# Kernel optimization log

Measured on AMD Instinct MI355X. Metric: run time of the kernel, lower is better.

The kernel has to match this reference:

```python
import jax, jax.numpy as jnp
import numpy as np

B, S, H, DH = 2, 4096, 8, 64
D = H * DH


def setup_inputs() -> dict:
    key = jax.random.key(0)
    ks = jax.random.split(key, 6)
    std = 1.0 / np.sqrt(D)
    return {
        "x": jax.random.normal(ks[0], (B, S, D), dtype=jnp.float32),
        "Wq": jax.random.normal(ks[1], (D, D), dtype=jnp.float32) * std,
        "Wk": jax.random.normal(ks[2], (D, D), dtype=jnp.float32) * std,
        "Wv": jax.random.normal(ks[3], (D, D), dtype=jnp.float32) * std,
        "Wo": jax.random.normal(ks[4], (D, D), dtype=jnp.float32) * std,
        "bo": jnp.zeros((D,), dtype=jnp.float32),
    }


def reference(x, Wq, Wk, Wv, Wo, bo):
    scale = DH ** (-0.5)
    # torch Linear: y = x @ W.T
    q = x @ Wq.T  # [B,S,D]
    k = x @ Wk.T
    v = x @ Wv.T
    # split heads -> [B,H,S,Dh]
    q = q.reshape(B, S, H, DH).transpose(0, 2, 1, 3)
    k = k.reshape(B, S, H, DH).transpose(0, 2, 1, 3)
    v = v.reshape(B, S, H, DH).transpose(0, 2, 1, 3)
    score = jnp.einsum('bhqd,bhkd->bhqk', q, k) * scale  # [B,H,S,S]
    weights = jax.nn.softmax(score, axis=-1)
    attn = jnp.einsum('bhqk,bhkd->bhqd', weights, v)  # [B,H,S,Dh]
    h_ = attn.transpose(0, 2, 1, 3).reshape(B, S, D)
    return h_ @ Wo.T + bo
```

## Files before the change

kernel.cpp:

```cpp
#include <hip/hip_runtime.h>

#define LOG2E 1.44269504088896340736f

typedef unsigned short u16;
typedef __bf16 bf16x4_t __attribute__((ext_vector_type(4)));
typedef __bf16 bf16x8_t __attribute__((ext_vector_type(8)));
typedef float f32x4_t __attribute__((ext_vector_type(4)));

__device__ __forceinline__ u16 f2bf(float f) {
  union { float f; unsigned int u; } v;
  v.f = f;
  unsigned int u = v.u;
  u += 0x7fffu + ((u >> 16) & 1u);
  return (u16)(u >> 16);
}

__device__ __forceinline__ f32x4_t mfma16(bf16x8_t a, bf16x8_t b, f32x4_t c) {
  return __builtin_amdgcn_mfma_f32_16x16x32_bf16(a, b, c, 0, 0, 0);
}

__device__ __forceinline__ void gl_lds16(const u16* g, u16* l) {
  __builtin_amdgcn_global_load_lds(
      (const __attribute__((address_space(1))) unsigned int*)g,
      (__attribute__((address_space(3))) unsigned int*)l, 16, 0, 0);
}

__global__ __launch_bounds__(256) void cast_all_kernel(
    const float* __restrict__ x, const float* __restrict__ wq, const float* __restrict__ wk,
    const float* __restrict__ wv, const float* __restrict__ wo,
    u16* __restrict__ xb, u16* __restrict__ wqb, u16* __restrict__ wkb,
    u16* __restrict__ wvb, u16* __restrict__ wob) {
  const int NX = 2 * 4096 * 512;
  const int NW = 512 * 512;
  int i = (blockIdx.x * 256 + threadIdx.x) * 4;
  const float* src; u16* dst; int off; float scale = 1.f;
  if (i < NX)               { src = x;  dst = xb;  off = i; }
  else if (i < NX + NW)     { src = wq; dst = wqb; off = i - NX; scale = 0.125f * LOG2E; }
  else if (i < NX + 2 * NW) { src = wk; dst = wkb; off = i - NX - NW; }
  else if (i < NX + 3 * NW) { src = wv; dst = wvb; off = i - NX - 2 * NW; }
  else                      { src = wo; dst = wob; off = i - NX - 3 * NW; }
  float4 f = *(const float4*)(src + off);
  unsigned int lo = (unsigned int)f2bf(f.x * scale) | ((unsigned int)f2bf(f.y * scale) << 16);
  unsigned int hi = (unsigned int)f2bf(f.z * scale) | ((unsigned int)f2bf(f.w * scale) << 16);
  uint2 o; o.x = lo; o.y = hi;
  *(uint2*)(dst + off) = o;
}

template <int MODE>
__device__ __forceinline__ void gemm_core(const u16* __restrict__ A, const u16* __restrict__ Bt,
                                          void* __restrict__ Cout, const float* __restrict__ bias,
                                          int Mbase, int Nbase) {
  __shared__ __align__(16) u16 As[128][40];
  __shared__ __align__(16) u16 Bs[128][40];
  const int t = threadIdx.x;
  const int wave = t >> 6, lane = t & 63;
  const int r = lane & 15, qd = lane >> 4;
  const int wm = wave & 1, wn = wave >> 1;
  const int lr = t >> 2;
  const int lc = (t & 3) * 8;

  f32x4_t acc[4][4];
#pragma unroll
  for (int i = 0; i < 4; i++)
#pragma unroll
    for (int j = 0; j < 4; j++) { f32x4_t z = {0.f, 0.f, 0.f, 0.f}; acc[i][j] = z; }

  for (int k0 = 0; k0 < 512; k0 += 32) {
    __syncthreads();
    *(uint4*)&As[lr][lc]      = *(const uint4*)(A  + (Mbase + lr) * 512 + k0 + lc);
    *(uint4*)&As[64 + lr][lc] = *(const uint4*)(A  + (Mbase + 64 + lr) * 512 + k0 + lc);
    *(uint4*)&Bs[lr][lc]      = *(const uint4*)(Bt + (Nbase + lr) * 512 + k0 + lc);
    *(uint4*)&Bs[64 + lr][lc] = *(const uint4*)(Bt + (Nbase + 64 + lr) * 512 + k0 + lc);
    __syncthreads();
    bf16x8_t af[4], bfr[4];
#pragma unroll
    for (int i = 0; i < 4; i++) af[i]  = *(const bf16x8_t*)&As[wm * 64 + i * 16 + r][qd * 8];
#pragma unroll
    for (int j = 0; j < 4; j++) bfr[j] = *(const bf16x8_t*)&Bs[wn * 64 + j * 16 + r][qd * 8];
#pragma unroll
    for (int i = 0; i < 4; i++)
#pragma unroll
      for (int j = 0; j < 4; j++) acc[i][j] = mfma16(af[i], bfr[j], acc[i][j]);
  }

  float bv[4];
  if (MODE == 2) {
#pragma unroll
    for (int j = 0; j < 4; j++) bv[j] = bias[Nbase + wn * 64 + j * 16 + r];
  }
#pragma unroll
  for (int i = 0; i < 4; i++) {
#pragma unroll
    for (int reg = 0; reg < 4; reg++) {
      int gr = Mbase + wm * 64 + i * 16 + qd * 4 + reg;
#pragma unroll
      for (int j = 0; j < 4; j++) {
        int gc = Nbase + wn * 64 + j * 16 + r;
        float val = acc[i][j][reg];
        if (MODE == 2) {
          ((float*)Cout)[gr * 512 + gc] = val + bv[j];
        } else if (MODE == 1) {
          int bb = gc >> 12, ss = gc & 4095;
          ((__bf16*)Cout)[((long)(bb * 512 + gr)) * 4096 + ss] = (__bf16)val;
        } else {
          ((__bf16*)Cout)[gr * 512 + gc] = (__bf16)val;
        }
      }
    }
  }
}

__global__ __launch_bounds__(256) void gemm_qkv_kernel(
    const u16* __restrict__ X,
    const u16* __restrict__ Wq, const u16* __restrict__ Wk, const u16* __restrict__ Wv,
    u16* __restrict__ Q, u16* __restrict__ K, u16* __restrict__ Vt) {
  if (blockIdx.z == 0)
    gemm_core<0>(X, Wq, Q, nullptr, blockIdx.x * 128, blockIdx.y * 128);
  else if (blockIdx.z == 1)
    gemm_core<0>(X, Wk, K, nullptr, blockIdx.x * 128, blockIdx.y * 128);
  else
    gemm_core<1>(Wv, X, Vt, nullptr, blockIdx.y * 128, blockIdx.x * 128);
}

__global__ __launch_bounds__(256) void gemm_out_kernel(
    const u16* __restrict__ Aat, const u16* __restrict__ Wo,
    float* __restrict__ Out, const float* __restrict__ bo) {
  gemm_core<2>(Aat, Wo, Out, bo, blockIdx.x * 128, blockIdx.y * 128);
}

__global__ __launch_bounds__(256, 2) void attn_kernel(
    const u16* __restrict__ Q, const u16* __restrict__ K, const u16* __restrict__ Vt,
    u16* __restrict__ Oattn) {
  __shared__ __align__(16) u16 Ks[2][4096];
  __shared__ __align__(16) u16 Vs[2][4096];
  __shared__ __align__(16) u16 Ps[4][4096];

  const int t = threadIdx.x;
  const int wave = t >> 6, lane = t & 63;
  const int r = lane & 15, qd = lane >> 4;
  const int g = wave & 1, kv = wave >> 1;
  const int bh = blockIdx.y;
  const int b = bh >> 3, h = bh & 7;
  const long bbase = (long)b * 4096 * 512;
  const int q0 = blockIdx.x * 128;

  const int sw = r & 7;
  const int ck0 = (qd ^ sw) * 8;
  const int ck1 = ((qd + 4) ^ sw) * 8;

  bf16x8_t qf[4][2];
#pragma unroll
  for (int qa = 0; qa < 4; qa++) {
    const u16* qp = Q + bbase + (long)(q0 + g * 64 + qa * 16 + r) * 512 + h * 64 + qd * 8;
    qf[qa][0] = *(const bf16x8_t*)(qp);
    qf[qa][1] = *(const bf16x8_t*)(qp + 32);
  }

  f32x4_t accO[4][4];
  float Lacc[4];
#pragma unroll
  for (int qa = 0; qa < 4; qa++) {
    f32x4_t z = {0.f, 0.f, 0.f, 0.f};
    Lacc[qa] = 0.f;
#pragma unroll
    for (int nt = 0; nt < 4; nt++) accO[qa][nt] = z;
  }

  const int rr = lane >> 3;
  const int cc = (lane & 7) ^ rr;
  const u16* kgb = K + bbase + (long)(kv * 2048 + g * 32 + rr) * 512 + h * 64 + cc * 8;
  const u16* vgb = Vt + ((long)(b * 512 + h * 64 + g * 32 + rr)) * 4096 + kv * 2048 + cc * 8;
  u16* kld = &Ks[kv][g * 32 * 64];
  u16* vld = &Vs[kv][g * 32 * 64];

  for (int k0 = 0; k0 < 2048; k0 += 64) {
    __syncthreads();
#pragma unroll
    for (int i = 0; i < 4; i++) gl_lds16(kgb + (long)k0 * 512 + i * 8 * 512, kld + i * 512);
#pragma unroll
    for (int i = 0; i < 4; i++) gl_lds16(vgb + k0 + i * 8 * 4096, vld + i * 512);
    __syncthreads();

    bf16x8_t kf[4][2];
#pragma unroll
    for (int nt = 0; nt < 4; nt++) {
      const u16* kb = &Ks[kv][(nt * 16 + r) * 64];
      kf[nt][0] = *(const bf16x8_t*)(kb + ck0);
      kf[nt][1] = *(const bf16x8_t*)(kb + ck1);
    }

    f32x4_t St[4][4];
#pragma unroll
    for (int qa = 0; qa < 4; qa++)
#pragma unroll
      for (int nt = 0; nt < 4; nt++) {
        f32x4_t z = {0.f, 0.f, 0.f, 0.f};
        z = mfma16(kf[nt][0], qf[qa][0], z);
        z = mfma16(kf[nt][1], qf[qa][1], z);
        St[qa][nt] = z;
      }

#pragma unroll
    for (int qa = 0; qa < 4; qa++) {
#pragma unroll
      for (int nt = 0; nt < 4; nt++) {
        float p0 = __builtin_amdgcn_exp2f(St[qa][nt][0]);
        float p1 = __builtin_amdgcn_exp2f(St[qa][nt][1]);
        float p2 = __builtin_amdgcn_exp2f(St[qa][nt][2]);
        float p3 = __builtin_amdgcn_exp2f(St[qa][nt][3]);
        Lacc[qa] += (p0 + p1) + (p2 + p3);
        bf16x4_t pk;
        pk[0] = (__bf16)p0; pk[1] = (__bf16)p1; pk[2] = (__bf16)p2; pk[3] = (__bf16)p3;
        int slot = (nt * 2 + (qd >> 1)) ^ sw;
        *(uint2*)&Ps[wave][(qa * 16 + r) * 64 + slot * 8 + (qd & 1) * 4] = *(uint2*)&pk;
      }
    }

    bf16x8_t pf[4][2];
#pragma unroll
    for (int qa = 0; qa < 4; qa++) {
      const u16* pb = &Ps[wave][(qa * 16 + r) * 64];
      pf[qa][0] = *(const bf16x8_t*)(pb + ck0);
      pf[qa][1] = *(const bf16x8_t*)(pb + ck1);
    }

#pragma unroll
    for (int nt = 0; nt < 4; nt++) {
      const u16* vb = &Vs[kv][(nt * 16 + r) * 64];
      bf16x8_t vf0 = *(const bf16x8_t*)(vb + ck0);
      bf16x8_t vf1 = *(const bf16x8_t*)(vb + ck1);
#pragma unroll
      for (int qa = 0; qa < 4; qa++) {
        accO[qa][nt] = mfma16(pf[qa][0], vf0, accO[qa][nt]);
        accO[qa][nt] = mfma16(pf[qa][1], vf1, accO[qa][nt]);
      }
    }
  }

  __syncthreads();
  float* Sc  = (float*)&Ps[0][0];
  float* Lsc = (float*)&Ks[0][0];
  if (kv == 1) {
#pragma unroll
    for (int qa = 0; qa < 4; qa++) {
#pragma unroll
      for (int nt = 0; nt < 4; nt++)
        *(f32x4_t*)&Sc[g * 4096 + ((qa * 4 + nt) * 64 + lane) * 4] = accO[qa][nt];
      Lsc[g * 256 + qa * 64 + lane] = Lacc[qa];
    }
  }
  __syncthreads();
  if (kv == 0) {
#pragma unroll
    for (int qa = 0; qa < 4; qa++) {
      Lacc[qa] += Lsc[g * 256 + qa * 64 + lane];
      float v = Lacc[qa];
      v += __shfl_xor(v, 16);
      v += __shfl_xor(v, 32);
      Lacc[qa] = v;
#pragma unroll
      for (int nt = 0; nt < 4; nt++) {
        f32x4_t o = *(const f32x4_t*)&Sc[g * 4096 + ((qa * 4 + nt) * 64 + lane) * 4];
        accO[qa][nt] += o;
      }
    }
#pragma unroll
    for (int qa = 0; qa < 4; qa++)
#pragma unroll
      for (int reg = 0; reg < 4; reg++) {
        float L = __shfl(Lacc[qa], qd * 4 + reg);
        float inv = 1.f / L;
        int gr = q0 + g * 64 + qa * 16 + qd * 4 + reg;
#pragma unroll
        for (int nt = 0; nt < 4; nt++)
          ((__bf16*)Oattn)[bbase + (long)gr * 512 + h * 64 + nt * 16 + r] =
              (__bf16)(accO[qa][nt][reg] * inv);
      }
  }
}

extern "C" void kernel_launch(void* const* d_in, const int* in_sizes, int n_in,
                              void* d_out, int out_size, void* d_ws, size_t ws_size,
                              hipStream_t stream) {
  const float* x  = (const float*)d_in[0];
  const float* Wq = (const float*)d_in[1];
  const float* Wk = (const float*)d_in[2];
  const float* Wv = (const float*)d_in[3];
  const float* Wo = (const float*)d_in[4];
  const float* bo = (const float*)d_in[5];
  float* out = (float*)d_out;

  u16* ws  = (u16*)d_ws;
  u16* xb  = ws;
  u16* wqb = xb  + 4194304;
  u16* wkb = wqb + 262144;
  u16* wvb = wkb + 262144;
  u16* wob = wvb + 262144;
  u16* Qb  = wob + 262144;
  u16* Kb  = Qb  + 4194304;
  u16* Vtg = Kb  + 4194304;
  u16* Ab  = Vtg + 4194304;

  cast_all_kernel<<<5120, 256, 0, stream>>>(x, Wq, Wk, Wv, Wo, xb, wqb, wkb, wvb, wob);

  dim3 g1(64, 4, 3);
  gemm_qkv_kernel<<<g1, 256, 0, stream>>>(xb, wqb, wkb, wvb, Qb, Kb, Vtg);

  dim3 g2(32, 16);
  attn_kernel<<<g2, 256, 0, stream>>>(Qb, Kb, Vtg, Ab);

  dim3 g3(64, 4);
  gemm_out_kernel<<<g3, 256, 0, stream>>>(Ab, wob, out, bo);
}
```

Before: 210.8 us.

## Double-buffer K/V tiles in attention and register-prefetch GEMM operands

The attention kernel now keeps two LDS buffers for the K and V tiles. It issues the async global-to-LDS loads for the next 64-key tile before computing on the current one, so there is one barrier per iteration instead of two. The per-wave P staging buffer is halved by writing and reading P in two 32-key halves interleaved with the PV MFMAs. The QKV and output GEMMs prefetch the next k-slice into registers while the current slice is multiplied from LDS. Together these aim to hide global load latency behind MFMA work. The cost is more LDS per block (80KB, still within two blocks per CU on 160KB) and more registers in the GEMM. Correctness depends on the async LDS loads having completed before the barrier.

```diff
diff --git a/kernel.cpp b/kernel.cpp
--- a/kernel.cpp
+++ b/kernel.cpp
@@ -65,22 +65,38 @@
 #pragma unroll
     for (int j = 0; j < 4; j++) { f32x4_t z = {0.f, 0.f, 0.f, 0.f}; acc[i][j] = z; }
 
+  const u16* pa0 = A  + (Mbase + lr) * 512 + lc;
+  const u16* pa1 = A  + (Mbase + 64 + lr) * 512 + lc;
+  const u16* pb0 = Bt + (Nbase + lr) * 512 + lc;
+  const u16* pb1 = Bt + (Nbase + 64 + lr) * 512 + lc;
+
+  uint4 ra0 = *(const uint4*)(pa0);
+  uint4 ra1 = *(const uint4*)(pa1);
+  uint4 rb0 = *(const uint4*)(pb0);
+  uint4 rb1 = *(const uint4*)(pb1);
+
   for (int k0 = 0; k0 < 512; k0 += 32) {
+    *(uint4*)&As[lr][lc]      = ra0;
+    *(uint4*)&As[64 + lr][lc] = ra1;
+    *(uint4*)&Bs[lr][lc]      = rb0;
+    *(uint4*)&Bs[64 + lr][lc] = rb1;
     __syncthreads();
-    *(uint4*)&As[lr][lc]      = *(const uint4*)(A  + (Mbase + lr) * 512 + k0 + lc);
-    *(uint4*)&As[64 + lr][lc] = *(const uint4*)(A  + (Mbase + 64 + lr) * 512 + k0 + lc);
-    *(uint4*)&Bs[lr][lc]      = *(const uint4*)(Bt + (Nbase + lr) * 512 + k0 + lc);
-    *(uint4*)&Bs[64 + lr][lc] = *(const uint4*)(Bt + (Nbase + 64 + lr) * 512 + k0 + lc);
+    if (k0 < 480) {
+      ra0 = *(const uint4*)(pa0 + k0 + 32);
+      ra1 = *(const uint4*)(pa1 + k0 + 32);
+      rb0 = *(const uint4*)(pb0 + k0 + 32);
+      rb1 = *(const uint4*)(pb1 + k0 + 32);
+    }
+    bf16x8_t af[4], bfr[4];
+#pragma unroll
+    for (int i = 0; i < 4; i++) af[i]  = *(const bf16x8_t*)&As[wm * 64 + i * 16 + r][qd * 8];
+#pragma unroll
+    for (int j = 0; j < 4; j++) bfr[j] = *(const bf16x8_t*)&Bs[wn * 64 + j * 16 + r][qd * 8];
+#pragma unroll
+    for (int i = 0; i < 4; i++)
+#pragma unroll
+      for (int j = 0; j < 4; j++) acc[i][j] = mfma16(af[i], bfr[j], acc[i][j]);
     __syncthreads();
-    bf16x8_t af[4], bfr[4];
-#pragma unroll
-    for (int i = 0; i < 4; i++) af[i]  = *(const bf16x8_t*)&As[wm * 64 + i * 16 + r][qd * 8];
-#pragma unroll
-    for (int j = 0; j < 4; j++) bfr[j] = *(const bf16x8_t*)&Bs[wn * 64 + j * 16 + r][qd * 8];
-#pragma unroll
-    for (int i = 0; i < 4; i++)
-#pragma unroll
-      for (int j = 0; j < 4; j++) acc[i][j] = mfma16(af[i], bfr[j], acc[i][j]);
   }
 
   float bv[4];
@@ -131,9 +147,9 @@
 __global__ __launch_bounds__(256, 2) void attn_kernel(
     const u16* __restrict__ Q, const u16* __restrict__ K, const u16* __restrict__ Vt,
     u16* __restrict__ Oattn) {
-  __shared__ __align__(16) u16 Ks[2][4096];
-  __shared__ __align__(16) u16 Vs[2][4096];
-  __shared__ __align__(16) u16 Ps[4][4096];
+  __shared__ __align__(16) u16 Ks[2][2][4096];
+  __shared__ __align__(16) u16 Vs[2][2][4096];
+  __shared__ __align__(16) u16 Ps[4][2048];
 
   const int t = threadIdx.x;
   const int wave = t >> 6, lane = t & 63;
@@ -147,6 +163,8 @@
   const int sw = r & 7;
   const int ck0 = (qd ^ sw) * 8;
   const int ck1 = ((qd + 4) ^ sw) * 8;
+  const int psw = r & 3;
+  const int pck = (qd ^ psw) * 8;
 
   bf16x8_t qf[4][2];
 #pragma unroll
@@ -170,21 +188,31 @@
   const int cc = (lane & 7) ^ rr;
   const u16* kgb = K + bbase + (long)(kv * 2048 + g * 32 + rr) * 512 + h * 64 + cc * 8;
   const u16* vgb = Vt + ((long)(b * 512 + h * 64 + g * 32 + rr)) * 4096 + kv * 2048 + cc * 8;
-  u16* kld = &Ks[kv][g * 32 * 64];
-  u16* vld = &Vs[kv][g * 32 * 64];
-
-  for (int k0 = 0; k0 < 2048; k0 += 64) {
+
+#pragma unroll
+  for (int i = 0; i < 4; i++) gl_lds16(kgb + (long)i * 8 * 512, &Ks[kv][0][g * 2048] + i * 512);
+#pragma unroll
+  for (int i = 0; i < 4; i++) gl_lds16(vgb + i * 8 * 4096, &Vs[kv][0][g * 2048] + i * 512);
+
+  for (int it = 0; it < 32; it++) {
+    const int buf = it & 1;
     __syncthreads();
-#pragma unroll
-    for (int i = 0; i < 4; i++) gl_lds16(kgb + (long)k0 * 512 + i * 8 * 512, kld + i * 512);
-#pragma unroll
-    for (int i = 0; i < 4; i++) gl_lds16(vgb + k0 + i * 8 * 4096, vld + i * 512);
-    __syncthreads();
+
+    if (it < 31) {
+      const int nb = (it + 1) & 1;
+      const long ko = (long)(it + 1) * 64;
+#pragma unroll
+      for (int i = 0; i < 4; i++)
+        gl_lds16(kgb + (ko + i * 8) * 512, &Ks[kv][nb][g * 2048] + i * 512);
+#pragma unroll
+      for (int i = 0; i < 4; i++)
+        gl_lds16(vgb + ko + (long)i * 8 * 4096, &Vs[kv][nb][g * 2048] + i * 512);
+    }
 
     bf16x8_t kf[4][2];
 #pragma unroll
     for (int nt = 0; nt < 4; nt++) {
-      const u16* kb = &Ks[kv][(nt * 16 + r) * 64];
+      const u16* kb = &Ks[kv][buf][(nt * 16 + r) * 64];
       kf[nt][0] = *(const bf16x8_t*)(kb + ck0);
       kf[nt][1] = *(const bf16x8_t*)(kb + ck1);
     }
@@ -200,8 +228,9 @@
         St[qa][nt] = z;
       }
 
-#pragma unroll
-    for (int qa = 0; qa < 4; qa++) {
+    bf16x4_t pk[4][4];
+#pragma unroll
+    for (int qa = 0; qa < 4; qa++)
 #pragma unroll
       for (int nt = 0; nt < 4; nt++) {
         float p0 = __builtin_amdgcn_exp2f(St[qa][nt][0]);
@@ -209,37 +238,38 @@
         float p2 = __builtin_amdgcn_exp2f(St[qa][nt][2]);
         float p3 = __builtin_amdgcn_exp2f(St[qa][nt][3]);
         Lacc[qa] += (p0 + p1) + (p2 + p3);
-        bf16x4_t pk;
-        pk[0] = (__bf16)p0; pk[1] = (__bf16)p1; pk[2] = (__bf16)p2; pk[3] = (__bf16)p3;
-        int slot = (nt * 2 + (qd >> 1)) ^ sw;
-        *(uint2*)&Ps[wave][(qa * 16 + r) * 64 + slot * 8 + (qd & 1) * 4] = *(uint2*)&pk;
-      }
-    }
-
-    bf16x8_t pf[4][2];
-#pragma unroll
-    for (int qa = 0; qa < 4; qa++) {
-      const u16* pb = &Ps[wave][(qa * 16 + r) * 64];
-      pf[qa][0] = *(const bf16x8_t*)(pb + ck0);
-      pf[qa][1] = *(const bf16x8_t*)(pb + ck1);
-    }
-
-#pragma unroll
-    for (int nt = 0; nt < 4; nt++) {
-      const u16* vb = &Vs[kv][(nt * 16 + r) * 64];
-      bf16x8_t vf0 = *(const bf16x8_t*)(vb + ck0);
-      bf16x8_t vf1 = *(const bf16x8_t*)(vb + ck1);
-#pragma unroll
-      for (int qa = 0; qa < 4; qa++) {
-        accO[qa][nt] = mfma16(pf[qa][0], vf0, accO[qa][nt]);
-        accO[qa][nt] = mfma16(pf[qa][1], vf1, accO[qa][nt]);
+        pk[qa][nt][0] = (__bf16)p0; pk[qa][nt][1] = (__bf16)p1;
+        pk[qa][nt][2] = (__bf16)p2; pk[qa][nt][3] = (__bf16)p3;
+      }
+
+#pragma unroll
+    for (int ks = 0; ks < 2; ks++) {
+#pragma unroll
+      for (int qa = 0; qa < 4; qa++)
+#pragma unroll
+        for (int nh = 0; nh < 2; nh++) {
+          int slot = ((nh * 2 + (qd >> 1)) ^ psw);
+          *(uint2*)&Ps[wave][(qa * 16 + r) * 32 + slot * 8 + (qd & 1) * 4] =
+              *(uint2*)&pk[qa][ks * 2 + nh];
+        }
+      bf16x8_t pf[4];
+#pragma unroll
+      for (int qa = 0; qa < 4; qa++)
+        pf[qa] = *(const bf16x8_t*)&Ps[wave][(qa * 16 + r) * 32 + pck];
+#pragma unroll
+      for (int nt = 0; nt < 4; nt++) {
+        const u16* vb = &Vs[kv][buf][(nt * 16 + r) * 64];
+        bf16x8_t vf = *(const bf16x8_t*)(vb + (ks ? ck1 : ck0));
+#pragma unroll
+        for (int qa = 0; qa < 4; qa++)
+          accO[qa][nt] = mfma16(pf[qa], vf, accO[qa][nt]);
       }
     }
   }
 
   __syncthreads();
-  float* Sc  = (float*)&Ps[0][0];
-  float* Lsc = (float*)&Ks[0][0];
+  float* Sc  = (float*)&Ks[0][0][0];
+  float* Lsc = (float*)&Vs[0][0][0];
   if (kv == 1) {
 #pragma unroll
     for (int qa = 0; qa < 4; qa++) {
```

Measured after the change: 211.5 us. No clear change (+0.3%).
